# Kernel tuning notes

Hardware: AMD Instinct MI355X
Metric: run time of the kernel (lower is better)

## Reference

```python
import jax, jax.numpy as jnp
import numpy as np

B, N, F, H, E, L = 4, 4096, 256, 256, 262144, 3
NTOT = B * N
EPS = 1e-5
NEG_SLOPE = 0.2  # PyG GATConv default leaky_relu slope


def setup_inputs() -> dict:
    key = jax.random.key(0)
    ks = jax.random.split(key, 10)
    s = 0.05
    return {
        "x": jax.random.normal(ks[0], (B, 1, N, F), jnp.float32),
        "edge_index": jax.random.randint(ks[1], (2, E), 0, NTOT, jnp.int64),
        "tc_w": jax.random.normal(ks[2], (H, F, 3), jnp.float32) * s,   # Conv1d weight [out,in,k]
        "tc_b": jax.random.normal(ks[3], (H,), jnp.float32) * s,
        "gat_W": jax.random.normal(ks[4], (L, H, H), jnp.float32) * s,  # per-layer lin weight (in==hidden)
        "gat_as": jax.random.normal(ks[5], (L, H), jnp.float32) * s,    # att_src
        "gat_ad": jax.random.normal(ks[6], (L, H), jnp.float32) * s,    # att_dst
        "gat_b": jax.random.normal(ks[7], (L, H), jnp.float32) * s,
        "ln_g": jnp.ones((H,), jnp.float32),
        "ln_b": jnp.zeros((H,), jnp.float32),
    }


def _gat_layer(h, W, a_s, a_d, b, src, dst):
    # h: [NTOT, H]; heads=1, eval mode (no dropout), self-loops already in src/dst
    hw = h @ W                                  # [NTOT, H]
    e = jax.nn.leaky_relu((hw @ a_s)[src] + (hw @ a_d)[dst], NEG_SLOPE)  # [E']
    m = jax.ops.segment_max(e, dst, num_segments=NTOT)
    ex = jnp.exp(e - m[dst])
    denom = jax.ops.segment_sum(ex, dst, num_segments=NTOT)
    alpha = ex / denom[dst]                     # edge softmax over incoming edges
    out = jax.ops.segment_sum(alpha[:, None] * hw[src], dst, num_segments=NTOT)
    return out + b


def reference(x, edge_index, tc_w, tc_b, gat_W, gat_as, gat_ad, gat_b, ln_g, ln_b):
    # add self loops (PyG GATConv default add_self_loops=True)
    loops = jnp.arange(NTOT, dtype=edge_index.dtype)
    src = jnp.concatenate([edge_index[0], loops])
    dst = jnp.concatenate([edge_index[1], loops])

    def conv1d(y):  # y: [B, C, N]
        o = jax.lax.conv_general_dilated(y, tc_w, (1,), [(1, 1)],
                                         dimension_numbers=("NCH", "OIH", "NCH"))
        return o + tc_b[None, :, None]

    xt = jnp.transpose(x[:, 0], (0, 2, 1))      # [B, F, N]
    xt = jax.nn.relu(conv1d(xt) + xt)           # temporal conv + residual

    h = jnp.transpose(xt, (0, 2, 1)).reshape(NTOT, H)
    for l in range(L):
        h = jax.nn.relu(_gat_layer(h, gat_W[l], gat_as[l], gat_ad[l], gat_b[l], src, dst))

    hg = jnp.transpose(h.reshape(B, N, H), (0, 2, 1))  # [B, H, N]
    out = conv1d(hg)[:, :, 0]                   # [B, H]

    mu = jnp.mean(out, axis=-1, keepdims=True)
    var = jnp.var(out, axis=-1, keepdims=True)
    out = (out - mu) / jnp.sqrt(var + EPS) * ln_g + ln_b
    return jax.nn.relu(out)
```

## Files before the change

### kernel.cpp

```cpp
#include <hip/hip_runtime.h>
#include <hip/hip_bf16.h>
#include <math.h>

#define NTOT 16384
#define HDIM 256
#define BBATCH 4
#define NSEQ 4096
#define FDIM 256
#define NE 262144
#define NEE (NE + NTOT)
#define NLAYER 3
#define LN_EPS 1e-5f
#define SLOPE 0.2f
#define CAP 64

typedef __attribute__((ext_vector_type(8))) short bf16x8;
typedef __attribute__((ext_vector_type(4))) float f32x4;

#define LDW 80
#define SLDW 72

#define OFF_HA   0u
#define OFF_HW   8388608u
#define OFF_WC   16777216u
#define OFF_WL   17170432u
#define OFF_SP   17563648u
#define OFF_DP   17825792u
#define OFF_CNT  18087936u
#define OFF_CSR  18153472u
#define OFF_WT   22347776u
#define OFF_F1   23134208u
#define OFF_F2   23199744u
#define OFF_L1   23265280u
#define OFF_L2   23330816u
#define OFF_CT   23396352u

static __device__ __forceinline__ unsigned short f2b(float f) {
    __hip_bfloat16 h = __float2bfloat16(f);
    return __builtin_bit_cast(unsigned short, h);
}
static __device__ __forceinline__ float b2f(unsigned short u) {
    __hip_bfloat16 h = __builtin_bit_cast(__hip_bfloat16, u);
    return __bfloat162float(h);
}
static __device__ __forceinline__ float rlanef(float v, int l) {
    return __builtin_bit_cast(float, __builtin_amdgcn_readlane(__builtin_bit_cast(int, v), l));
}

static __device__ __forceinline__ void wave_append(bool isNew, int src, int lane,
                                                   int* ctp, int* list) {
    unsigned long long mask = __ballot(isNew);
    int base = 0;
    if (lane == 0 && mask) base = atomicAdd(ctp, (int)__popcll(mask));
    base = __shfl(base, 0);
    if (isNew) {
        int off = (int)__popcll(mask & ((1ull << lane) - 1ull));
        list[base + off] = src;
    }
}

__global__ __launch_bounds__(256) void k_pre(const float* __restrict__ tcw, const float* __restrict__ gatW,
                                             unsigned short* __restrict__ wcB, unsigned short* __restrict__ WTb,
                                             float* __restrict__ wT, int* __restrict__ cnt,
                                             int* __restrict__ flag1, int* __restrict__ flag2,
                                             int* __restrict__ ct) {
    int b = blockIdx.x, t = threadIdx.x;
    if (b < 256) {
        const float* s = tcw + b * 768 + t * 3;
        wcB[b * 768 + 0 + t]   = f2b(s[0]);
        wcB[b * 768 + 256 + t] = f2b(s[1]);
        wcB[b * 768 + 512 + t] = f2b(s[2]);
    } else if (b < 1024) {
        int ln = b - 256; int n = ln & 255; int l = ln >> 8;
        WTb[(size_t)l * 65536 + n * 256 + t] = f2b(gatW[(size_t)l * 65536 + t * 256 + n]);
    } else if (b < 1792) {
        int fk = b - 1024; int f = fk / 3, k = fk - 3 * f;
        wT[(k * FDIM + f) * HDIM + t] = tcw[t * 768 + fk];
    } else if (b < 1808) {
        int i = ((b - 1792) * 256 + t) * 4;
        *(int4*)(cnt + i) = make_int4(0, 0, 0, 0);
    } else if (b < 1824) {
        int i = ((b - 1808) * 256 + t) * 4;
        *(int4*)(flag1 + i) = make_int4(0, 0, 0, 0);
    } else if (b < 1840) {
        int i = ((b - 1824) * 256 + t) * 4;
        *(int4*)(flag2 + i) = make_int4(0, 0, 0, 0);
    } else {
        if (t < 2) ct[t] = 0;
    }
}

__global__ __launch_bounds__(256) void k_conv(const float* __restrict__ x,
                                              const unsigned short* __restrict__ wcB,
                                              const float* __restrict__ tcb,
                                              unsigned short* __restrict__ hAb,
                                              const int* __restrict__ ei, int* __restrict__ cnt,
                                              int* __restrict__ csr,
                                              int* __restrict__ flag2, int* __restrict__ list2,
                                              int* __restrict__ ct) {
    __shared__ char slab[130 * SLDW];
    __shared__ char Bs[3 * 64 * LDW];
    int t = threadIdx.x;
    if (blockIdx.x >= 128) {
        int cid = (blockIdx.x - 128) * 4 + blockIdx.y;
        int e = cid * 256 + t;
        int src, dst;
        if (e < NE) { src = ei[e]; dst = ei[NE + e]; } else { src = dst = e - NE; }
        int slot = atomicAdd(&cnt[dst], 1);
        if (slot < CAP) csr[dst * CAP + slot] = src;
        bool isNew = false;
        if ((dst & 4095) < 2) isNew = (atomicExch(&flag2[src], 1) == 0);
        wave_append(isNew, src, t & 63, &ct[0], list2);
        return;
    }
    int m0 = blockIdx.x * 128, n0 = blockIdx.y * 64;
    int bb = m0 >> 12;
    int nloc0 = m0 & 4095;
    int w = t >> 6, lane = t & 63;
    int wr = w >> 1, wc = w & 1;
    int row16 = lane & 15, kg = lane >> 4;
    int rA = t >> 1, hh = t & 1;
    f32x4 acc[4][2];
    #pragma unroll
    for (int mi = 0; mi < 4; ++mi)
        #pragma unroll
        for (int ni = 0; ni < 2; ++ni) acc[mi][ni] = (f32x4)(0.f);

    for (int kb = 0; kb < 8; ++kb) {
        int c0 = kb * 32;
        __syncthreads();
        {
            int nl = nloc0 - 1 + rA;
            ushort4 o0 = make_ushort4(0,0,0,0), o1 = make_ushort4(0,0,0,0),
                    o2 = make_ushort4(0,0,0,0), o3 = make_ushort4(0,0,0,0);
            if ((unsigned)nl < 4096u) {
// ... 35 lines not shown
            #pragma unroll
            for (int ni = 0; ni < 2; ++ni)
                bfr[ni] = *(bf16x8*)&Bs[p * 64 * LDW + (wc * 32 + ni * 16 + row16) * LDW + kg * 16];
            #pragma unroll
            for (int mi = 0; mi < 4; ++mi) {
                bf16x8 afr = *(bf16x8*)&slab[(wr * 64 + mi * 16 + row16 + p) * SLDW + kg * 16];
                acc[mi][0] = __builtin_amdgcn_mfma_f32_16x16x32_bf16(afr, bfr[0], acc[mi][0], 0, 0, 0);
                acc[mi][1] = __builtin_amdgcn_mfma_f32_16x16x32_bf16(afr, bfr[1], acc[mi][1], 0, 0, 0);
            }
        }
    }
    #pragma unroll
    for (int mi = 0; mi < 4; ++mi)
        #pragma unroll
        for (int ni = 0; ni < 2; ++ni) {
            int rowl = wr * 64 + mi * 16 + kg * 4;
            int coll = wc * 32 + ni * 16 + row16;
            int n = n0 + coll;
            float bc = tcb[n];
            #pragma unroll
            for (int q = 0; q < 4; ++q) {
                size_t node = (size_t)(m0 + rowl + q);
                float v = acc[mi][ni][q] + bc + x[node * 256 + n];
                v = v > 0.f ? v : 0.f;
                hAb[node * 256 + n] = f2b(v);
            }
        }
}

__global__ __launch_bounds__(256) void k_gemm_layer(const unsigned short* __restrict__ hAb,
                                                    const unsigned short* __restrict__ WT,
                                                    const float* __restrict__ as, const float* __restrict__ ad,
                                                    unsigned short* __restrict__ hwB,
                                                    float* __restrict__ sPart, float* __restrict__ dPart,
                                                    const int* __restrict__ cnt, const int* __restrict__ csr,
                                                    int* __restrict__ flag1,
                                                    int* __restrict__ list1, const int* __restrict__ list2,
                                                    int* __restrict__ ct) {
    __shared__ char lds[128 * LDW + 64 * LDW];
    __shared__ float sRed[256], dRed[256];
    char* As = lds;
    char* Bs = lds + 128 * LDW;
    int t = threadIdx.x;
    if (blockIdx.x == 128) {
        int lane = t & 63;
        int n2 = ct[0];
        int total = n2 * CAP;
        for (int p = blockIdx.y * 256 + t; p < total; p += 1024) {
            int node = list2[p >> 6];
            int j = p & (CAP - 1);
            int src = 0; bool isNew = false;
            if (j < cnt[node]) {
                src = csr[node * CAP + j];
                isNew = (atomicExch(&flag1[src], 1) == 0);
            }
            wave_append(isNew, src, lane, &ct[1], list1);
        }
        return;
    }
    int m0 = blockIdx.x * 128, n0 = blockIdx.y * 64;
    int w = t >> 6, lane = t & 63;
    int wr = w >> 1, wc = w & 1;
    int row16 = lane & 15, kg = lane >> 4;
    int rA = t >> 1, hh = t & 1;
    f32x4 acc[4][2];
    #pragma unroll
    for (int mi = 0; mi < 4; ++mi)
        #pragma unroll
        for (int ni = 0; ni < 2; ++ni) acc[mi][ni] = (f32x4)(0.f);

    for (int kb = 0; kb < 256; kb += 32) {
        {
            const uint4* src = (const uint4*)(hAb + (size_t)(m0 + rA) * 256 + kb + hh * 16);
            uint4 v0 = src[0], v1 = src[1];
            *(uint4*)&As[rA * LDW + hh * 32] = v0;
            *(uint4*)&As[rA * LDW + hh * 32 + 16] = v1;
        }
        if (t < 128) {
            int rB = t >> 1;
            const uint4* src = (const uint4*)(WT + (size_t)(n0 + rB) * 256 + kb + hh * 16);
            uint4 v0 = src[0], v1 = src[1];
            *(uint4*)&Bs[rB * LDW + hh * 32] = v0;
            *(uint4*)&Bs[rB * LDW + hh * 32 + 16] = v1;
        }
        __syncthreads();
        bf16x8 bfr[2];
        #pragma unroll
        for (int ni = 0; ni < 2; ++ni)
            bfr[ni] = *(bf16x8*)&Bs[(wc * 32 + ni * 16 + row16) * LDW + kg * 16];
        #pragma unroll
        for (int mi = 0; mi < 4; ++mi) {
            bf16x8 afr = *(bf16x8*)&As[(wr * 64 + mi * 16 + row16) * LDW + kg * 16];
            acc[mi][0] = __builtin_amdgcn_mfma_f32_16x16x32_bf16(afr, bfr[0], acc[mi][0], 0, 0, 0);
            acc[mi][1] = __builtin_amdgcn_mfma_f32_16x16x32_bf16(afr, bfr[1], acc[mi][1], 0, 0, 0);
        }
        __syncthreads();
    }
    #pragma unroll
    for (int mi = 0; mi < 4; ++mi)
        #pragma unroll
        for (int ni = 0; ni < 2; ++ni) {
            int rowl = wr * 64 + mi * 16 + kg * 4;
            int coll = wc * 32 + ni * 16 + row16;
            size_t base = (size_t)(m0 + rowl) * 256 + n0 + coll;
            #pragma unroll
            for (int q = 0; q < 4; ++q) hwB[base + (size_t)q * 256] = f2b(acc[mi][ni][q]);
        }
    float asv0 = as[n0 + wc * 32 + row16];
    float asv1 = as[n0 + wc * 32 + 16 + row16];
    float adv0 = ad[n0 + wc * 32 + row16];
    float adv1 = ad[n0 + wc * 32 + 16 + row16];
    #pragma unroll
    for (int mi = 0; mi < 4; ++mi)
        #pragma unroll
        for (int q = 0; q < 4; ++q) {
            float ps = acc[mi][0][q] * asv0 + acc[mi][1][q] * asv1;
            float pd = acc[mi][0][q] * adv0 + acc[mi][1][q] * adv1;
            #pragma unroll
            for (int o = 1; o < 16; o <<= 1) { ps += __shfl_xor(ps, o); pd += __shfl_xor(pd, o); }
            if (row16 == 0) {
                int rowl = wr * 64 + mi * 16 + kg * 4 + q;
                sRed[rowl * 2 + wc] = ps;
                dRed[rowl * 2 + wc] = pd;
            }
        }
    __syncthreads();
    if (t < 128) {
        sPart[(size_t)blockIdx.y * NTOT + m0 + t] = sRed[t * 2] + sRed[t * 2 + 1];
        dPart[(size_t)blockIdx.y * NTOT + m0 + t] = dRed[t * 2] + dRed[t * 2 + 1];
    }
}

__global__ __launch_bounds__(256) void k_gemm_list(const unsigned short* __restrict__ hAb,
                                                   const unsigned short* __restrict__ WT,
                                                   const float* __restrict__ as, const float* __restrict__ ad,
                                                   unsigned short* __restrict__ hwB,
                                                   float* __restrict__ sPart, float* __restrict__ dPart,
                                                   const int* __restrict__ list, const int* __restrict__ cptr) {
    __shared__ char lds[128 * LDW + 64 * LDW];
    __shared__ float sRed[256], dRed[256];
    __shared__ int rows[128];
    char* As = lds;
    char* Bs = lds + 128 * LDW;
    int t = threadIdx.x;
    int n = *cptr;
    int m0 = blockIdx.x * 128;
    if (m0 >= n) return;
    int n0 = blockIdx.y * 64;
    if (t < 128) {
        int idx = m0 + t;
        rows[t] = list[idx < n ? idx : n - 1];
    }
    __syncthreads();
    int w = t >> 6, lane = t & 63;
    int wr = w >> 1, wc = w & 1;
    int row16 = lane & 15, kg = lane >> 4;
    int rA = t >> 1, hh = t & 1;
    f32x4 acc[4][2];
    #pragma unroll
    for (int mi = 0; mi < 4; ++mi)
        #pragma unroll
        for (int ni = 0; ni < 2; ++ni) acc[mi][ni] = (f32x4)(0.f);

    for (int kb = 0; kb < 256; kb += 32) {
        {
            const uint4* src = (const uint4*)(hAb + (size_t)rows[rA] * 256 + kb + hh * 16);
            uint4 v0 = src[0], v1 = src[1];
            *(uint4*)&As[rA * LDW + hh * 32] = v0;
            *(uint4*)&As[rA * LDW + hh * 32 + 16] = v1;
        }
        if (t < 128) {
            int rB = t >> 1;
            const uint4* src = (const uint4*)(WT + (size_t)(n0 + rB) * 256 + kb + hh * 16);
            uint4 v0 = src[0], v1 = src[1];
            *(uint4*)&Bs[rB * LDW + hh * 32] = v0;
            *(uint4*)&Bs[rB * LDW + hh * 32 + 16] = v1;
        }
        __syncthreads();
        bf16x8 bfr[2];
        #pragma unroll
        for (int ni = 0; ni < 2; ++ni)
            bfr[ni] = *(bf16x8*)&Bs[(wc * 32 + ni * 16 + row16) * LDW + kg * 16];
        #pragma unroll
        for (int mi = 0; mi < 4; ++mi) {
            bf16x8 afr = *(bf16x8*)&As[(wr * 64 + mi * 16 + row16) * LDW + kg * 16];
            acc[mi][0] = __builtin_amdgcn_mfma_f32_16x16x32_bf16(afr, bfr[0], acc[mi][0], 0, 0, 0);
            acc[mi][1] = __builtin_amdgcn_mfma_f32_16x16x32_bf16(afr, bfr[1], acc[mi][1], 0, 0, 0);
        }
        __syncthreads();
    }
    #pragma unroll
    for (int mi = 0; mi < 4; ++mi)
        #pragma unroll
        for (int ni = 0; ni < 2; ++ni) {
            int rowl = wr * 64 + mi * 16 + kg * 4;
            int coll = wc * 32 + ni * 16 + row16;
            #pragma unroll
            for (int q = 0; q < 4; ++q)
                hwB[(size_t)rows[rowl + q] * 256 + n0 + coll] = f2b(acc[mi][ni][q]);
        }
    float asv0 = as[n0 + wc * 32 + row16];
    float asv1 = as[n0 + wc * 32 + 16 + row16];
    float adv0 = ad[n0 + wc * 32 + row16];
    float adv1 = ad[n0 + wc * 32 + 16 + row16];
    #pragma unroll
    for (int mi = 0; mi < 4; ++mi)
        #pragma unroll
        for (int q = 0; q < 4; ++q) {
            float ps = acc[mi][0][q] * asv0 + acc[mi][1][q] * asv1;
            float pd = acc[mi][0][q] * adv0 + acc[mi][1][q] * adv1;
            #pragma unroll
            for (int o = 1; o < 16; o <<= 1) { ps += __shfl_xor(ps, o); pd += __shfl_xor(pd, o); }
            if (row16 == 0) {
                int rowl = wr * 64 + mi * 16 + kg * 4 + q;
                sRed[rowl * 2 + wc] = ps;
                dRed[rowl * 2 + wc] = pd;
            }
        }
    __syncthreads();
    if (t < 128) {
        int node = rows[t];
        sPart[(size_t)blockIdx.y * NTOT + node] = sRed[t * 2] + sRed[t * 2 + 1];
        dPart[(size_t)blockIdx.y * NTOT + node] = dRed[t * 2] + dRed[t * 2 + 1];
    }
}

__global__ __launch_bounds__(256) void k_agg_list(const unsigned short* __restrict__ hwB,
                                                  const float* __restrict__ sPart, const float* __restrict__ dPart,
                                                  const int* __restrict__ cnt, const int* __restrict__ csr,
                                                  const float* __restrict__ bias,
                                                  unsigned short* __restrict__ hout,
                                                  const int* __restrict__ list, const int* __restrict__ cptr) {
    int tid = threadIdx.x;
    int wave = tid >> 6, lane = tid & 63;
    int n = *cptr;
    const ushort4* hw4 = (const ushort4*)hwB;
    for (int idx = blockIdx.x * 4 + wave; idx < n; idx += gridDim.x * 4) {
        int node = list[idx];
        int deg = cnt[node];
        const int* bucket = csr + node * CAP;
        float di = dPart[node] + dPart[NTOT + node] + dPart[2 * NTOT + node] + dPart[3 * NTOT + node];
        float denom = 0.f;
        float a0 = 0.f, a1 = 0.f, a2 = 0.f, a3 = 0.f;
        for (int cb = 0; cb < deg; cb += 64) {
            int j = cb + lane;
            int sj = 0;
            float myw = 0.f;
            if (j < deg) {
                sj = bucket[j];
                float sv = sPart[sj] + sPart[NTOT + sj] + sPart[2 * NTOT + sj] + sPart[3 * NTOT + sj];
                float e = sv + di;
                e = e > 0.f ? e : SLOPE * e;
                myw = __expf(e);
            }
            float csum = myw;
            #pragma unroll
            for (int o = 1; o < 64; o <<= 1) csum += __shfl_xor(csum, o);
            denom += csum;
            int c = deg - cb; if (c > 64) c = 64;
            int q = 0;
            for (; q + 8 <= c; q += 8) {
                int si[8]; float wi[8]; ushort4 vv[8];
                #pragma unroll
                for (int u = 0; u < 8; ++u) {
                    si[u] = __builtin_amdgcn_readlane(sj, q + u);
                    wi[u] = rlanef(myw, q + u);
                }
                #pragma unroll
                for (int u = 0; u < 8; ++u) vv[u] = hw4[(size_t)si[u] * 64 + lane];
                #pragma unroll
                for (int u = 0; u < 8; ++u) {
                    a0 = fmaf(wi[u], b2f(vv[u].x), a0);
                    a1 = fmaf(wi[u], b2f(vv[u].y), a1);
                    a2 = fmaf(wi[u], b2f(vv[u].z), a2);
                    a3 = fmaf(wi[u], b2f(vv[u].w), a3);
                }
            }
            if (q < c) {
                int rem = c - q;
                int si[8]; float wi[8]; ushort4 vv[8];
                #pragma unroll
                for (int u = 0; u < 8; ++u) {
                    int qq = q + (u < rem ? u : 0);
                    si[u] = __builtin_amdgcn_readlane(sj, qq);
                    wi[u] = (u < rem) ? rlanef(myw, qq) : 0.f;
                }
                #pragma unroll
                for (int u = 0; u < 8; ++u) vv[u] = hw4[(size_t)si[u] * 64 + lane];
                #pragma unroll
                for (int u = 0; u < 8; ++u) {
                    a0 = fmaf(wi[u], b2f(vv[u].x), a0);
                    a1 = fmaf(wi[u], b2f(vv[u].y), a1);
                    a2 = fmaf(wi[u], b2f(vv[u].z), a2);
                    a3 = fmaf(wi[u], b2f(vv[u].w), a3);
                }
            }
        }
        float inv = 1.f / denom;
        float4 bb = ((const float4*)bias)[lane];
        ushort4 o;
        float o0 = a0 * inv + bb.x; o.x = f2b(o0 > 0.f ? o0 : 0.f);
        float o1 = a1 * inv + bb.y; o.y = f2b(o1 > 0.f ? o1 : 0.f);
        float o2 = a2 * inv + bb.z; o.z = f2b(o2 > 0.f ? o2 : 0.f);
        float o3 = a3 * inv + bb.w; o.w = f2b(o3 > 0.f ? o3 : 0.f);
        ((ushort4*)hout)[(size_t)node * 64 + lane] = o;
    }
}

__global__ __launch_bounds__(256) void k_aggfinal(const unsigned short* __restrict__ hwB,
                                                  const float* __restrict__ sPart, const float* __restrict__ dPart,
                                                  const int* __restrict__ cnt, const int* __restrict__ csr,
                                                  const float* __restrict__ bias,
                                                  const float* __restrict__ wT, const float* __restrict__ tcb,
                                                  const float* __restrict__ g, const float* __restrict__ bln,
                                                  float* __restrict__ out) {
    __shared__ float r01[2][HDIM];
    __shared__ float red[16];
    int b = blockIdx.x, t = threadIdx.x;
    int w = t >> 6, lane = t & 63;
    if (w < 2) {
        int node = b * NSEQ + w;
        int deg = cnt[node];
        const int* bucket = csr + node * CAP;
        float di = dPart[node] + dPart[NTOT + node] + dPart[2 * NTOT + node] + dPart[3 * NTOT + node];
        const ushort4* hw4 = (const ushort4*)hwB;
        float denom = 0.f;
        float a0 = 0.f, a1 = 0.f, a2 = 0.f, a3 = 0.f;
        for (int cb = 0; cb < deg; cb += 64) {
            int j = cb + lane;
            int sj = 0;
            float myw = 0.f;
            if (j < deg) {
                sj = bucket[j];
                float sv = sPart[sj] + sPart[NTOT + sj] + sPart[2 * NTOT + sj] + sPart[3 * NTOT + sj];
                float e = sv + di;
                e = e > 0.f ? e : SLOPE * e;
                myw = __expf(e);
            }
            float csum = myw;
            #pragma unroll
            for (int o = 1; o < 64; o <<= 1) csum += __shfl_xor(csum, o);
            denom += csum;
            int c = deg - cb; if (c > 64) c = 64;
            for (int q = 0; q < c; ++q) {
                int sq = __builtin_amdgcn_readlane(sj, q);
                float wq = rlanef(myw, q);
                ushort4 v = hw4[(size_t)sq * 64 + lane];
                a0 = fmaf(wq, b2f(v.x), a0); a1 = fmaf(wq, b2f(v.y), a1);
                a2 = fmaf(wq, b2f(v.z), a2); a3 = fmaf(wq, b2f(v.w), a3);
            }
        }
        float inv = 1.f / denom;
        float4 bb = ((const float4*)bias)[lane];
        float o0 = a0 * inv + bb.x;
        float o1 = a1 * inv + bb.y;
        float o2 = a2 * inv + bb.z;
        float o3 = a3 * inv + bb.w;
        r01[w][lane * 4 + 0] = o0 > 0.f ? o0 : 0.f;
        r01[w][lane * 4 + 1] = o1 > 0.f ? o1 : 0.f;
        r01[w][lane * 4 + 2] = o2 > 0.f ? o2 : 0.f;
        r01[w][lane * 4 + 3] = o3 > 0.f ? o3 : 0.f;
    }
    __syncthreads();
    int c = t;
    float a = tcb[c];
    for (int f = 0; f < FDIM; ++f) {
        a = fmaf(wT[(1 * FDIM + f) * HDIM + c], r01[0][f], a);
        a = fmaf(wT[(2 * FDIM + f) * HDIM + c], r01[1][f], a);
    }
    float ss = a, sq = a * a;
    #pragma unroll
    for (int o = 1; o < 64; o <<= 1) { ss += __shfl_xor(ss, o); sq += __shfl_xor(sq, o); }
    if (lane == 0) { red[w] = ss; red[8 + w] = sq; }
    __syncthreads();
    float tot = 0.f, totq = 0.f;
    #pragma unroll
    for (int u = 0; u < 4; ++u) { tot += red[u]; totq += red[8 + u]; }
    float mu = tot * (1.f / HDIM);
    float var = totq * (1.f / HDIM) - mu * mu;
    float v = (a - mu) * rsqrtf(var + LN_EPS) * g[c] + bln[c];
    out[b * HDIM + c] = v > 0.f ? v : 0.f;
}

extern "C" void kernel_launch(void* const* d_in, const int* in_sizes, int n_in,
                              void* d_out, int out_size, void* d_ws, size_t ws_size,
                              hipStream_t stream) {
    const float* x     = (const float*)d_in[0];
    const int*   ei    = (const int*)d_in[1];
    const float* tcw   = (const float*)d_in[2];
    const float* tcb   = (const float*)d_in[3];
    const float* gatW  = (const float*)d_in[4];
    const float* gatas = (const float*)d_in[5];
    const float* gatad = (const float*)d_in[6];
    const float* gatb  = (const float*)d_in[7];
    const float* lng   = (const float*)d_in[8];
    const float* lnb   = (const float*)d_in[9];
    float* out = (float*)d_out;

    char* ws = (char*)d_ws;
    unsigned short* hAb = (unsigned short*)(ws + OFF_HA);
    unsigned short* hwB = (unsigned short*)(ws + OFF_HW);
    unsigned short* wcB = (unsigned short*)(ws + OFF_WC);
    unsigned short* WTb = (unsigned short*)(ws + OFF_WL);
    float* sPart = (float*)(ws + OFF_SP);
    float* dPart = (float*)(ws + OFF_DP);
    int*   cnt  = (int*)(ws + OFF_CNT);
    int*   csr  = (int*)(ws + OFF_CSR);
    float* wT   = (float*)(ws + OFF_WT);
    int*   flag1 = (int*)(ws + OFF_F1);
    int*   flag2 = (int*)(ws + OFF_F2);
    int*   list1 = (int*)(ws + OFF_L1);
    int*   list2 = (int*)(ws + OFF_L2);
    int*   ct    = (int*)(ws + OFF_CT);

    k_pre<<<1841, 256, 0, stream>>>(tcw, gatW, wcB, WTb, wT, cnt, flag1, flag2, ct);
    k_conv<<<dim3(128 + 272, 4), 256, 0, stream>>>(x, wcB, tcb, hAb, ei, cnt, csr,
                                                   flag2, list2, ct);

    k_gemm_layer<<<dim3(129, 4), 256, 0, stream>>>(
        hAb, WTb, gatas, gatad, hwB, sPart, dPart,
        cnt, csr, flag1, list1, list2, ct);
    k_agg_list<<<1024, 256, 0, stream>>>(hwB, sPart, dPart, cnt, csr, gatb, hAb, list1, ct + 1);

    k_gemm_list<<<dim3(128, 4), 256, 0, stream>>>(
        hAb, WTb + 65536, gatas + HDIM, gatad + HDIM, hwB, sPart, dPart, list1, ct + 1);
    k_agg_list<<<128, 256, 0, stream>>>(hwB, sPart, dPart, cnt, csr, gatb + HDIM, hAb, list2, ct);

    k_gemm_list<<<dim3(4, 4), 256, 0, stream>>>(
        hAb, WTb + 131072, gatas + 2 * HDIM, gatad + 2 * HDIM, hwB, sPart, dPart, list2, ct);
    k_aggfinal<<<BBATCH, 256, 0, stream>>>(hwB, sPart, dPart, cnt, csr, gatb + 2 * HDIM,
                                           wT, tcb, lng, lnb, out);
}
```

Before: 117.5 us.

## Fuse GAT tail layers into one cooperative kernel with grid syncs

Replaces the chain of per-layer aggregation and list-GEMM kernels, plus the final aggregation and LayerNorm kernel, with a single cooperative kernel of 256 blocks. The stages inside it are separated by grid.sync, and aggregation and GEMM work is spread over the list entries with grid-stride loops. Weight transposes and the flag1 clear move from the prep kernel into spare blocks of the conv kernel, and the layer-0 GEMM no longer builds the second frontier list. The intent is to remove kernel launch gaps and tail latency on the small frontier stages. In exchange, building list1 is no longer overlapped with the layer-0 GEMM, and each grid-wide barrier adds its own cost.

```diff
diff --git a/kernel.cpp b/kernel.cpp
--- a/kernel.cpp
+++ b/kernel.cpp
@@ -1,6 +1,9 @@
 #include <hip/hip_runtime.h>
 #include <hip/hip_bf16.h>
+#include <hip/hip_cooperative_groups.h>
 #include <math.h>
+
+namespace cg = cooperative_groups;
 
 #define NTOT 16384
 #define HDIM 256
@@ -9,7 +12,6 @@
 #define FDIM 256
 #define NE 262144
 #define NEE (NE + NTOT)
-#define NLAYER 3
 #define LN_EPS 1e-5f
 #define SLOPE 0.2f
 #define CAP 64
@@ -59,10 +61,182 @@
     }
 }
 
-__global__ __launch_bounds__(256) void k_pre(const float* __restrict__ tcw, const float* __restrict__ gatW,
-                                             unsigned short* __restrict__ wcB, unsigned short* __restrict__ WTb,
-                                             float* __restrict__ wT, int* __restrict__ cnt,
-                                             int* __restrict__ flag1, int* __restrict__ flag2,
+static __device__ __forceinline__ float4 agg_node(const unsigned short* __restrict__ hwB,
+                                                  const float* __restrict__ sPart,
+                                                  const float* __restrict__ dPart,
+                                                  const int* __restrict__ cnt,
+                                                  const int* __restrict__ csr,
+                                                  const float* __restrict__ bias,
+                                                  int node, int lane) {
+    int deg = cnt[node];
+    const int* bucket = csr + node * CAP;
+    float di = dPart[node] + dPart[NTOT + node] + dPart[2 * NTOT + node] + dPart[3 * NTOT + node];
+    const ushort4* hw4 = (const ushort4*)hwB;
+    float denom = 0.f;
+    float a0 = 0.f, a1 = 0.f, a2 = 0.f, a3 = 0.f;
+    for (int cb = 0; cb < deg; cb += 64) {
+        int j = cb + lane;
+        int sj = 0;
+        float myw = 0.f;
+        if (j < deg) {
+            sj = bucket[j];
+            float sv = sPart[sj] + sPart[NTOT + sj] + sPart[2 * NTOT + sj] + sPart[3 * NTOT + sj];
+            float e = sv + di;
+            e = e > 0.f ? e : SLOPE * e;
+            myw = __expf(e);
+        }
+        float csum = myw;
+        #pragma unroll
+        for (int o = 1; o < 64; o <<= 1) csum += __shfl_xor(csum, o);
+        denom += csum;
+        int c = deg - cb; if (c > 64) c = 64;
+        int q = 0;
+        for (; q + 8 <= c; q += 8) {
+            int si[8]; float wi[8]; ushort4 vv[8];
+            #pragma unroll
+            for (int u = 0; u < 8; ++u) {
+                si[u] = __builtin_amdgcn_readlane(sj, q + u);
+                wi[u] = rlanef(myw, q + u);
+            }
+            #pragma unroll
+            for (int u = 0; u < 8; ++u) vv[u] = hw4[(size_t)si[u] * 64 + lane];
+            #pragma unroll
+            for (int u = 0; u < 8; ++u) {
+                a0 = fmaf(wi[u], b2f(vv[u].x), a0);
+                a1 = fmaf(wi[u], b2f(vv[u].y), a1);
+                a2 = fmaf(wi[u], b2f(vv[u].z), a2);
+                a3 = fmaf(wi[u], b2f(vv[u].w), a3);
+            }
+        }
+        if (q < c) {
+            int rem = c - q;
+            int si[8]; float wi[8]; ushort4 vv[8];
+            #pragma unroll
+            for (int u = 0; u < 8; ++u) {
+                int qq = q + (u < rem ? u : 0);
+                si[u] = __builtin_amdgcn_readlane(sj, qq);
+                wi[u] = (u < rem) ? rlanef(myw, qq) : 0.f;
+            }
+            #pragma unroll
+            for (int u = 0; u < 8; ++u) vv[u] = hw4[(size_t)si[u] * 64 + lane];
+            #pragma unroll
+            for (int u = 0; u < 8; ++u) {
+                a0 = fmaf(wi[u], b2f(vv[u].x), a0);
+                a1 = fmaf(wi[u], b2f(vv[u].y), a1);
+                a2 = fmaf(wi[u], b2f(vv[u].z), a2);
+                a3 = fmaf(wi[u], b2f(vv[u].w), a3);
+            }
+        }
+    }
+    float inv = 1.f / denom;
+    float4 bb = ((const float4*)bias)[lane];
+    float4 o;
+    o.x = a0 * inv + bb.x; o.x = o.x > 0.f ? o.x : 0.f;
+    o.y = a1 * inv + bb.y; o.y = o.y > 0.f ? o.y : 0.f;
+    o.z = a2 * inv + bb.z; o.z = o.z > 0.f ? o.z : 0.f;
+    o.w = a3 * inv + bb.w; o.w = o.w > 0.f ? o.w : 0.f;
+    return o;
+}
+
+static __device__ __forceinline__ void gemm_tile(const unsigned short* __restrict__ hAb,
+                                                 const unsigned short* __restrict__ WT,
+                                                 const float* __restrict__ as, const float* __restrict__ ad,
+                                                 unsigned short* __restrict__ hwB,
+                                                 float* __restrict__ sPart, float* __restrict__ dPart,
+                                                 const int* __restrict__ list, int n, int m0, int n0,
+                                                 char* As, char* Bs, float* sRed, float* dRed, int* rows) {
+    int t = threadIdx.x;
+    __syncthreads();
+    if (t < 128) {
+        int idx = m0 + t;
+        rows[t] = list[idx < n ? idx : n - 1];
+    }
+    __syncthreads();
+    int w = t >> 6, lane = t & 63;
+    int wr = w >> 1, wc = w & 1;
+    int row16 = lane & 15, kg = lane >> 4;
+    int rA = t >> 1, hh = t & 1;
+    f32x4 acc[4][2];
+    #pragma unroll
+    for (int mi = 0; mi < 4; ++mi)
+        #pragma unroll
+        for (int ni = 0; ni < 2; ++ni) acc[mi][ni] = (f32x4)(0.f);
+
+    for (int kb = 0; kb < 256; kb += 32) {
+        {
+            const uint4* src = (const uint4*)(hAb + (size_t)rows[rA] * 256 + kb + hh * 16);
+            uint4 v0 = src[0], v1 = src[1];
+            *(uint4*)&As[rA * LDW + hh * 32] = v0;
+            *(uint4*)&As[rA * LDW + hh * 32 + 16] = v1;
+        }
+        if (t < 128) {
+            int rB = t >> 1;
+            const uint4* src = (const uint4*)(WT + (size_t)(n0 + rB) * 256 + kb + hh * 16);
+            uint4 v0 = src[0], v1 = src[1];
+            *(uint4*)&Bs[rB * LDW + hh * 32] = v0;
+            *(uint4*)&Bs[rB * LDW + hh * 32 + 16] = v1;
+        }
+        __syncthreads();
+        bf16x8 bfr[2];
+        #pragma unroll
+        for (int ni = 0; ni < 2; ++ni)
+            bfr[ni] = *(bf16x8*)&Bs[(wc * 32 + ni * 16 + row16) * LDW + kg * 16];
+        #pragma unroll
+        for (int mi = 0; mi < 4; ++mi) {
+            bf16x8 afr = *(bf16x8*)&As[(wr * 64 + mi * 16 + row16) * LDW + kg * 16];
+            acc[mi][0] = __builtin_amdgcn_mfma_f32_16x16x32_bf16(afr, bfr[0], acc[mi][0], 0, 0, 0);
+            acc[mi][1] = __builtin_amdgcn_mfma_f32_16x16x32_bf16(afr, bfr[1], acc[mi][1], 0, 0, 0);
+        }
+        __syncthreads();
+    }
+    #pragma unroll
+    for (int mi = 0; mi < 4; ++mi)
+        #pragma unroll
+        for (int ni = 0; ni < 2; ++ni) {
+            int rowl = wr * 64 + mi * 16 + kg * 4;
+            int coll = wc * 32 + ni * 16 + row16;
+            #pragma unroll
+            for (int q = 0; q < 4; ++q)
+                hwB[(size_t)rows[rowl + q] * 256 + n0 + coll] = f2b(acc[mi][ni][q]);
+        }
+    float asv0 = as[n0 + wc * 32 + row16];
+    float asv1 = as[n0 + wc * 32 + 16 + row16];
+    float adv0 = ad[n0 + wc * 32 + row16];
+    float adv1 = ad[n0 + wc * 32 + 16 + row16];
+    #pragma unroll
+    for (int mi = 0; mi < 4; ++mi)
+        #pragma unroll
+        for (int q = 0; q < 4; ++q) {
+            float ps = acc[mi][0][q] * asv0 + acc[mi][1][q] * asv1;
+            float pd = acc[mi][0][q] * adv0 + acc[mi][1][q] * adv1;
+            #pragma unroll
+            for (int o = 1; o < 16; o <<= 1) { ps += __shfl_xor(ps, o); pd += __shfl_xor(pd, o); }
+            if (row16 == 0) {
+                int rowl = wr * 64 + mi * 16 + kg * 4 + q;
+                sRed[rowl * 2 + wc] = ps;
+                dRed[rowl * 2 + wc] = pd;
+            }
+        }
+    __syncthreads();
+    if (t < 128) {
+        int node = rows[t];
+        sPart[(size_t)blockIdx.y * 0 + 0 * NTOT + node] = sRed[t * 2] + sRed[t * 2 + 1];
+        dPart[node] = dRed[t * 2] + dRed[t * 2 + 1];
+    }
+}
+
+static __device__ __forceinline__ void gemm_tile_sd(const unsigned short* hAb, const unsigned short* WT,
+                                                    const float* as, const float* ad,
+                                                    unsigned short* hwB, float* sPart, float* dPart,
+                                                    const int* list, int n, int m0, int n0,
+                                                    char* As, char* Bs, float* sRed, float* dRed, int* rows) {
+    gemm_tile(hAb, WT, as, ad, hwB, sPart + (size_t)(n0 >> 6) * NTOT, dPart + (size_t)(n0 >> 6) * NTOT,
+              list, n, m0, n0, As, Bs, sRed, dRed, rows);
+}
+
+__global__ __launch_bounds__(256) void k_pre(const float* __restrict__ tcw,
+                                             unsigned short* __restrict__ wcB,
+                                             int* __restrict__ cnt, int* __restrict__ flag2,
                                              int* __restrict__ ct) {
     int b = blockIdx.x, t = threadIdx.x;
     if (b < 256) {
@@ -70,20 +244,11 @@
         wcB[b * 768 + 0 + t]   = f2b(s[0]);
         wcB[b * 768 + 256 + t] = f2b(s[1]);
         wcB[b * 768 + 512 + t] = f2b(s[2]);
-    } else if (b < 1024) {
-        int ln = b - 256; int n = ln & 255; int l = ln >> 8;
-        WTb[(size_t)l * 65536 + n * 256 + t] = f2b(gatW[(size_t)l * 65536 + t * 256 + n]);
-    } else if (b < 1792) {
-        int fk = b - 1024; int f = fk / 3, k = fk - 3 * f;
-        wT[(k * FDIM + f) * HDIM + t] = tcw[t * 768 + fk];
-    } else if (b < 1808) {
-        int i = ((b - 1792) * 256 + t) * 4;
+    } else if (b < 272) {
+        int i = ((b - 256) * 256 + t) * 4;
         *(int4*)(cnt + i) = make_int4(0, 0, 0, 0);
-    } else if (b < 1824) {
-        int i = ((b - 1808) * 256 + t) * 4;
-        *(int4*)(flag1 + i) = make_int4(0, 0, 0, 0);
-    } else if (b < 1840) {
-        int i = ((b - 1824) * 256 + t) * 4;
+    } else if (b < 288) {
+        int i = ((b - 272) * 256 + t) * 4;
         *(int4*)(flag2 + i) = make_int4(0, 0, 0, 0);
     } else {
         if (t < 2) ct[t] = 0;
@@ -97,10 +262,27 @@
                                               const int* __restrict__ ei, int* __restrict__ cnt,
                                               int* __restrict__ csr,
                                               int* __restrict__ flag2, int* __restrict__ list2,
-                                              int* __restrict__ ct) {
+                                              int* __restrict__ ct,
+                                              const float* __restrict__ tcw, const float* __restrict__ gatW,
+                                              unsigned short* __restrict__ WTb, float* __restrict__ wT,
+                                              int* __restrict__ flag1) {
     __shared__ char slab[130 * SLDW];
     __shared__ char Bs[3 * 64 * LDW];
     int t = threadIdx.x;
+    if (blockIdx.x >= 400) {
+        int pid = (blockIdx.x - 400) * 4 + blockIdx.y;
+        if (pid < 768) {
+            int l = pid >> 8, n = pid & 255;
+            WTb[(size_t)l * 65536 + n * 256 + t] = f2b(gatW[(size_t)l * 65536 + t * 256 + n]);
+        } else if (pid < 1536) {
+            int fk = pid - 768; int f = fk / 3, k = fk - 3 * f;
+            wT[(k * FDIM + f) * HDIM + t] = tcw[t * 768 + fk];
+        } else {
+            int i = ((pid - 1536) * 256 + t) * 4;
+            *(int4*)(flag1 + i) = make_int4(0, 0, 0, 0);
+        }
+        return;
+    }
     if (blockIdx.x >= 128) {
         int cid = (blockIdx.x - 128) * 4 + blockIdx.y;
         int e = cid * 256 + t;
@@ -202,21 +384,108 @@
                                                     const unsigned short* __restrict__ WT,
                                                     const float* __restrict__ as, const float* __restrict__ ad,
                                                     unsigned short* __restrict__ hwB,
-                                                    float* __restrict__ sPart, float* __restrict__ dPart,
-                                                    const int* __restrict__ cnt, const int* __restrict__ csr,
-                                                    int* __restrict__ flag1,
-                                                    int* __restrict__ list1, const int* __restrict__ list2,
-                                                    int* __restrict__ ct) {
+                                                    float* __restrict__ sPart, float* __restrict__ dPart) {
     __shared__ char lds[128 * LDW + 64 * LDW];
     __shared__ float sRed[256], dRed[256];
     char* As = lds;
     char* Bs = lds + 128 * LDW;
     int t = threadIdx.x;
-    if (blockIdx.x == 128) {
-        int lane = t & 63;
+    int m0 = blockIdx.x * 128, n0 = blockIdx.y * 64;
+    int w = t >> 6, lane = t & 63;
+    int wr = w >> 1, wc = w & 1;
+    int row16 = lane & 15, kg = lane >> 4;
+    int rA = t >> 1, hh = t & 1;
+    f32x4 acc[4][2];
+    #pragma unroll
+    for (int mi = 0; mi < 4; ++mi)
+        #pragma unroll
+        for (int ni = 0; ni < 2; ++ni) acc[mi][ni] = (f32x4)(0.f);
+
+    for (int kb = 0; kb < 256; kb += 32) {
+        {
+            const uint4* src = (const uint4*)(hAb + (size_t)(m0 + rA) * 256 + kb + hh * 16);
+            uint4 v0 = src[0], v1 = src[1];
+            *(uint4*)&As[rA * LDW + hh * 32] = v0;
+            *(uint4*)&As[rA * LDW + hh * 32 + 16] = v1;
+        }
+        if (t < 128) {
+            int rB = t >> 1;
+            const uint4* src = (const uint4*)(WT + (size_t)(n0 + rB) * 256 + kb + hh * 16);
+            uint4 v0 = src[0], v1 = src[1];
+            *(uint4*)&Bs[rB * LDW + hh * 32] = v0;
+            *(uint4*)&Bs[rB * LDW + hh * 32 + 16] = v1;
+        }
+        __syncthreads();
+        bf16x8 bfr[2];
+        #pragma unroll
+        for (int ni = 0; ni < 2; ++ni)
+            bfr[ni] = *(bf16x8*)&Bs[(wc * 32 + ni * 16 + row16) * LDW + kg * 16];
+        #pragma unroll
+        for (int mi = 0; mi < 4; ++mi) {
+            bf16x8 afr = *(bf16x8*)&As[(wr * 64 + mi * 16 + row16) * LDW + kg * 16];
+            acc[mi][0] = __builtin_amdgcn_mfma_f32_16x16x32_bf16(afr, bfr[0], acc[mi][0], 0, 0, 0);
+            acc[mi][1] = __builtin_amdgcn_mfma_f32_16x16x32_bf16(afr, bfr[1], acc[mi][1], 0, 0, 0);
+        }
+        __syncthreads();
+    }
+    #pragma unroll
+    for (int mi = 0; mi < 4; ++mi)
+        #pragma unroll
+        for (int ni = 0; ni < 2; ++ni) {
+            int rowl = wr * 64 + mi * 16 + kg * 4;
+            int coll = wc * 32 + ni * 16 + row16;
+            size_t base = (size_t)(m0 + rowl) * 256 + n0 + coll;
+            #pragma unroll
+            for (int q = 0; q < 4; ++q) hwB[base + (size_t)q * 256] = f2b(acc[mi][ni][q]);
+        }
+    float asv0 = as[n0 + wc * 32 + row16];
+    float asv1 = as[n0 + wc * 32 + 16 + row16];
+    float adv0 = ad[n0 + wc * 32 + row16];
+    float adv1 = ad[n0 + wc * 32 + 16 + row16];
+    #pragma unroll
+    for (int mi = 0; mi < 4; ++mi)
+        #pragma unroll
+        for (int q = 0; q < 4; ++q) {
+            float ps = acc[mi][0][q] * asv0 + acc[mi][1][q] * asv1;
+            float pd = acc[mi][0][q] * adv0 + acc[mi][1][q] * adv1;
+            #pragma unroll
+            for (int o = 1; o < 16; o <<= 1) { ps += __shfl_xor(ps, o); pd += __shfl_xor(pd, o); }
+            if (row16 == 0) {
+                int rowl = wr * 64 + mi * 16 + kg * 4 + q;
+                sRed[rowl * 2 + wc] = ps;
+                dRed[rowl * 2 + wc] = pd;
+            }
+        }
+    __syncthreads();
+    if (t < 128) {
+        sPart[(size_t)blockIdx.y * NTOT + m0 + t] = sRed[t * 2] + sRed[t * 2 + 1];
+        dPart[(size_t)blockIdx.y * NTOT + m0 + t] = dRed[t * 2] + dRed[t * 2 + 1];
+    }
+}
+
+__global__ __launch_bounds__(256) void k_tail(unsigned short* hAb, unsigned short* hwB,
+                                              const unsigned short* WTb,
+                                              const float* gatas, const float* gatad, const float* gatb,
+                                              float* sPart, float* dPart,
+                                              const int* cnt, const int* csr,
+                                              int* flag1, int* list1, const int* list2, int* ct,
+                                              const float* wT, const float* tcb,
+                                              const float* g, const float* bln, float* out) {
+    cg::grid_group grid = cg::this_grid();
+    __shared__ char As[128 * LDW];
+    __shared__ char Bs[64 * LDW];
+    __shared__ float sRed[256], dRed[256];
+    __shared__ int rows[128];
+    __shared__ float r01[2][HDIM];
+    __shared__ float red[16];
+    int b = blockIdx.x, t = threadIdx.x;
+    int wv = t >> 6, lane = t & 63;
+    int nb = gridDim.x;
+
+    if (b < 4) {
         int n2 = ct[0];
         int total = n2 * CAP;
-        for (int p = blockIdx.y * 256 + t; p < total; p += 1024) {
+        for (int p = b * 256 + t; p < total; p += 1024) {
             int node = list2[p >> 6];
             int j = p & (CAP - 1);
             int src = 0; bool isNew = false;
@@ -226,330 +495,74 @@
             }
             wave_append(isNew, src, lane, &ct[1], list1);
         }
-        return;
-    }
-    int m0 = blockIdx.x * 128, n0 = blockIdx.y * 64;
-    int w = t >> 6, lane = t & 63;
-    int wr = w >> 1, wc = w & 1;
-    int row16 = lane & 15, kg = lane >> 4;
-    int rA = t >> 1, hh = t & 1;
-    f32x4 acc[4][2];
-    #pragma unroll
-    for (int mi = 0; mi < 4; ++mi)
-        #pragma unroll
-        for (int ni = 0; ni < 2; ++ni) acc[mi][ni] = (f32x4)(0.f);
-
-    for (int kb = 0; kb < 256; kb += 32) {
-        {
-            const uint4* src = (const uint4*)(hAb + (size_t)(m0 + rA) * 256 + kb + hh * 16);
-            uint4 v0 = src[0], v1 = src[1];
-            *(uint4*)&As[rA * LDW + hh * 32] = v0;
-            *(uint4*)&As[rA * LDW + hh * 32 + 16] = v1;
-        }
-        if (t < 128) {
-            int rB = t >> 1;
-            const uint4* src = (const uint4*)(WT + (size_t)(n0 + rB) * 256 + kb + hh * 16);
-            uint4 v0 = src[0], v1 = src[1];
-            *(uint4*)&Bs[rB * LDW + hh * 32] = v0;
-            *(uint4*)&Bs[rB * LDW + hh * 32 + 16] = v1;
-        }
-        __syncthreads();
-        bf16x8 bfr[2];
-        #pragma unroll
-        for (int ni = 0; ni < 2; ++ni)
-            bfr[ni] = *(bf16x8*)&Bs[(wc * 32 + ni * 16 + row16) * LDW + kg * 16];
-        #pragma unroll
-        for (int mi = 0; mi < 4; ++mi) {
-            bf16x8 afr = *(bf16x8*)&As[(wr * 64 + mi * 16 + row16) * LDW + kg * 16];
-            acc[mi][0] = __builtin_amdgcn_mfma_f32_16x16x32_bf16(afr, bfr[0], acc[mi][0], 0, 0, 0);
-            acc[mi][1] = __builtin_amdgcn_mfma_f32_16x16x32_bf16(afr, bfr[1], acc[mi][1], 0, 0, 0);
-        }
-        __syncthreads();
-    }
-    #pragma unroll
-    for (int mi = 0; mi < 4; ++mi)
-        #pragma unroll
-        for (int ni = 0; ni < 2; ++ni) {
-            int rowl = wr * 64 + mi * 16 + kg * 4;
-            int coll = wc * 32 + ni * 16 + row16;
-            size_t base = (size_t)(m0 + rowl) * 256 + n0 + coll;
-            #pragma unroll
-            for (int q = 0; q < 4; ++q) hwB[base + (size_t)q * 256] = f2b(acc[mi][ni][q]);
-        }
-    float asv0 = as[n0 + wc * 32 + row16];
-    float asv1 = as[n0 + wc * 32 + 16 + row16];
-    float adv0 = ad[n0 + wc * 32 + row16];
-    float adv1 = ad[n0 + wc * 32 + 16 + row16];
-    #pragma unroll
-    for (int mi = 0; mi < 4; ++mi)
-        #pragma unroll
-        for (int q = 0; q < 4; ++q) {
-            float ps = acc[mi][0][q] * asv0 + acc[mi][1][q] * asv1;
-            float pd = acc[mi][0][q] * adv0 + acc[mi][1][q] * adv1;
-            #pragma unroll
-            for (int o = 1; o < 16; o <<= 1) { ps += __shfl_xor(ps, o); pd += __shfl_xor(pd, o); }
-            if (row16 == 0) {
-                int rowl = wr * 64 + mi * 16 + kg * 4 + q;
-                sRed[rowl * 2 + wc] = ps;
-                dRed[rowl * 2 + wc] = pd;
-            }
-        }
-    __syncthreads();
-    if (t < 128) {
-        sPart[(size_t)blockIdx.y * NTOT + m0 + t] = sRed[t * 2] + sRed[t * 2 + 1];
-        dPart[(size_t)blockIdx.y * NTOT + m0 + t] = dRed[t * 2] + dRed[t * 2 + 1];
-    }
-}
-
-__global__ __launch_bounds__(256) void k_gemm_list(const unsigned short* __restrict__ hAb,
-                                                   const unsigned short* __restrict__ WT,
-                                                   const float* __restrict__ as, const float* __restrict__ ad,
-                                                   unsigned short* __restrict__ hwB,
-                                                   float* __restrict__ sPart, float* __restrict__ dPart,
-                                                   const int* __restrict__ list, const int* __restrict__ cptr) {
-    __shared__ char lds[128 * LDW + 64 * LDW];
-    __shared__ float sRed[256], dRed[256];
-    __shared__ int rows[128];
-    char* As = lds;
-    char* Bs = lds + 128 * LDW;
-    int t = threadIdx.x;
-    int n = *cptr;
-    int m0 = blockIdx.x * 128;
-    if (m0 >= n) return;
-    int n0 = blockIdx.y * 64;
-    if (t < 128) {
-        int idx = m0 + t;
-        rows[t] = list[idx < n ? idx : n - 1];
-    }
-    __syncthreads();
-    int w = t >> 6, lane = t & 63;
-    int wr = w >> 1, wc = w & 1;
-    int row16 = lane & 15, kg = lane >> 4;
-    int rA = t >> 1, hh = t & 1;
-    f32x4 acc[4][2];
-    #pragma unroll
-    for (int mi = 0; mi < 4; ++mi)
-        #pragma unroll
-        for (int ni = 0; ni < 2; ++ni) acc[mi][ni] = (f32x4)(0.f);
-
-    for (int kb = 0; kb < 256; kb += 32) {
-        {
-            const uint4* src = (const uint4*)(hAb + (size_t)rows[rA] * 256 + kb + hh * 16);
-            uint4 v0 = src[0], v1 = src[1];
-            *(uint4*)&As[rA * LDW + hh * 32] = v0;
-            *(uint4*)&As[rA * LDW + hh * 32 + 16] = v1;
-        }
-        if (t < 128) {
-            int rB = t >> 1;
-            const uint4* src = (const uint4*)(WT + (size_t)(n0 + rB) * 256 + kb + hh * 16);
-            uint4 v0 = src[0], v1 = src[1];
-            *(uint4*)&Bs[rB * LDW + hh * 32] = v0;
-            *(uint4*)&Bs[rB * LDW + hh * 32 + 16] = v1;
-        }
-        __syncthreads();
-        bf16x8 bfr[2];
-        #pragma unroll
-        for (int ni = 0; ni < 2; ++ni)
-            bfr[ni] = *(bf16x8*)&Bs[(wc * 32 + ni * 16 + row16) * LDW + kg * 16];
-        #pragma unroll
-        for (int mi = 0; mi < 4; ++mi) {
-            bf16x8 afr = *(bf16x8*)&As[(wr * 64 + mi * 16 + row16) * LDW + kg * 16];
-            acc[mi][0] = __builtin_amdgcn_mfma_f32_16x16x32_bf16(afr, bfr[0], acc[mi][0], 0, 0, 0);
-            acc[mi][1] = __builtin_amdgcn_mfma_f32_16x16x32_bf16(afr, bfr[1], acc[mi][1], 0, 0, 0);
-        }
-        __syncthreads();
-    }
-    #pragma unroll
-    for (int mi = 0; mi < 4; ++mi)
-        #pragma unroll
-        for (int ni = 0; ni < 2; ++ni) {
-            int rowl = wr * 64 + mi * 16 + kg * 4;
-            int coll = wc * 32 + ni * 16 + row16;
-            #pragma unroll
-            for (int q = 0; q < 4; ++q)
-                hwB[(size_t)rows[rowl + q] * 256 + n0 + coll] = f2b(acc[mi][ni][q]);
-        }
-    float asv0 = as[n0 + wc * 32 + row16];
-    float asv1 = as[n0 + wc * 32 + 16 + row16];
-    float adv0 = ad[n0 + wc * 32 + row16];
-    float adv1 = ad[n0 + wc * 32 + 16 + row16];
-    #pragma unroll
-    for (int mi = 0; mi < 4; ++mi)
-        #pragma unroll
-        for (int q = 0; q < 4; ++q) {
-            float ps = acc[mi][0][q] * asv0 + acc[mi][1][q] * asv1;
-            float pd = acc[mi][0][q] * adv0 + acc[mi][1][q] * adv1;
-            #pragma unroll
-            for (int o = 1; o < 16; o <<= 1) { ps += __shfl_xor(ps, o); pd += __shfl_xor(pd, o); }
-            if (row16 == 0) {
-                int rowl = wr * 64 + mi * 16 + kg * 4 + q;
-                sRed[rowl * 2 + wc] = ps;
-                dRed[rowl * 2 + wc] = pd;
-            }
-        }
-    __syncthreads();
-    if (t < 128) {
-        int node = rows[t];
-        sPart[(size_t)blockIdx.y * NTOT + node] = sRed[t * 2] + sRed[t * 2 + 1];
-        dPart[(size_t)blockIdx.y * NTOT + node] = dRed[t * 2] + dRed[t * 2 + 1];
-    }
-}
-
-__global__ __launch_bounds__(256) void k_agg_list(const unsigned short* __restrict__ hwB,
-                                                  const float* __restrict__ sPart, const float* __restrict__ dPart,
-                                                  const int* __restrict__ cnt, const int* __restrict__ csr,
-                                                  const float* __restrict__ bias,
-                                                  unsigned short* __restrict__ hout,
-                                                  const int* __restrict__ list, const int* __restrict__ cptr) {
-    int tid = threadIdx.x;
-    int wave = tid >> 6, lane = tid & 63;
-    int n = *cptr;
-    const ushort4* hw4 = (const ushort4*)hwB;
-    for (int idx = blockIdx.x * 4 + wave; idx < n; idx += gridDim.x * 4) {
-        int node = list[idx];
-        int deg = cnt[node];
-        const int* bucket = csr + node * CAP;
-        float di = dPart[node] + dPart[NTOT + node] + dPart[2 * NTOT + node] + dPart[3 * NTOT + node];
-        float denom = 0.f;
-        float a0 = 0.f, a1 = 0.f, a2 = 0.f, a3 = 0.f;
-        for (int cb = 0; cb < deg; cb += 64) {
-            int j = cb + lane;
-            int sj = 0;
-            float myw = 0.f;
-            if (j < deg) {
-                sj = bucket[j];
-                float sv = sPart[sj] + sPart[NTOT + sj] + sPart[2 * NTOT + sj] + sPart[3 * NTOT + sj];
-                float e = sv + di;
-                e = e > 0.f ? e : SLOPE * e;
-                myw = __expf(e);
-            }
-            float csum = myw;
-            #pragma unroll
-            for (int o = 1; o < 64; o <<= 1) csum += __shfl_xor(csum, o);
-            denom += csum;
-            int c = deg - cb; if (c > 64) c = 64;
-            int q = 0;
-            for (; q + 8 <= c; q += 8) {
-                int si[8]; float wi[8]; ushort4 vv[8];
-                #pragma unroll
-                for (int u = 0; u < 8; ++u) {
-                    si[u] = __builtin_amdgcn_readlane(sj, q + u);
-                    wi[u] = rlanef(myw, q + u);
-                }
-                #pragma unroll
-                for (int u = 0; u < 8; ++u) vv[u] = hw4[(size_t)si[u] * 64 + lane];
-                #pragma unroll
-                for (int u = 0; u < 8; ++u) {
-                    a0 = fmaf(wi[u], b2f(vv[u].x), a0);
-                    a1 = fmaf(wi[u], b2f(vv[u].y), a1);
-                    a2 = fmaf(wi[u], b2f(vv[u].z), a2);
-                    a3 = fmaf(wi[u], b2f(vv[u].w), a3);
-                }
-            }
-            if (q < c) {
-                int rem = c - q;
-                int si[8]; float wi[8]; ushort4 vv[8];
-                #pragma unroll
-                for (int u = 0; u < 8; ++u) {
-                    int qq = q + (u < rem ? u : 0);
-                    si[u] = __builtin_amdgcn_readlane(sj, qq);
-                    wi[u] = (u < rem) ? rlanef(myw, qq) : 0.f;
-                }
-                #pragma unroll
-                for (int u = 0; u < 8; ++u) vv[u] = hw4[(size_t)si[u] * 64 + lane];
-                #pragma unroll
-                for (int u = 0; u < 8; ++u) {
-                    a0 = fmaf(wi[u], b2f(vv[u].x), a0);
-                    a1 = fmaf(wi[u], b2f(vv[u].y), a1);
-                    a2 = fmaf(wi[u], b2f(vv[u].z), a2);
-                    a3 = fmaf(wi[u], b2f(vv[u].w), a3);
-                }
-            }
-        }
-        float inv = 1.f / denom;
-        float4 bb = ((const float4*)bias)[lane];
-        ushort4 o;
-        float o0 = a0 * inv + bb.x; o.x = f2b(o0 > 0.f ? o0 : 0.f);
-        float o1 = a1 * inv + bb.y; o.y = f2b(o1 > 0.f ? o1 : 0.f);
-        float o2 = a2 * inv + bb.z; o.z = f2b(o2 > 0.f ? o2 : 0.f);
-        float o3 = a3 * inv + bb.w; o.w = f2b(o3 > 0.f ? o3 : 0.f);
-        ((ushort4*)hout)[(size_t)node * 64 + lane] = o;
-    }
-}
-
-__global__ __launch_bounds__(256) void k_aggfinal(const unsigned short* __restrict__ hwB,
-                                                  const float* __restrict__ sPart, const float* __restrict__ dPart,
-                                                  const int* __restrict__ cnt, const int* __restrict__ csr,
-                                                  const float* __restrict__ bias,
-                                                  const float* __restrict__ wT, const float* __restrict__ tcb,
-                                                  const float* __restrict__ g, const float* __restrict__ bln,
-                                                  float* __restrict__ out) {
-    __shared__ float r01[2][HDIM];
-    __shared__ float red[16];
-    int b = blockIdx.x, t = threadIdx.x;
-    int w = t >> 6, lane = t & 63;
-    if (w < 2) {
-        int node = b * NSEQ + w;
-        int deg = cnt[node];
-        const int* bucket = csr + node * CAP;
-        float di = dPart[node] + dPart[NTOT + node] + dPart[2 * NTOT + node] + dPart[3 * NTOT + node];
-        const ushort4* hw4 = (const ushort4*)hwB;
-        float denom = 0.f;
-        float a0 = 0.f, a1 = 0.f, a2 = 0.f, a3 = 0.f;
-        for (int cb = 0; cb < deg; cb += 64) {
-            int j = cb + lane;
-            int sj = 0;
-            float myw = 0.f;
-            if (j < deg) {
-                sj = bucket[j];
-                float sv = sPart[sj] + sPart[NTOT + sj] + sPart[2 * NTOT + sj] + sPart[3 * NTOT + sj];
-                float e = sv + di;
-                e = e > 0.f ? e : SLOPE * e;
-                myw = __expf(e);
-            }
-            float csum = myw;
-            #pragma unroll
-            for (int o = 1; o < 64; o <<= 1) csum += __shfl_xor(csum, o);
-            denom += csum;
-            int c = deg - cb; if (c > 64) c = 64;
-            for (int q = 0; q < c; ++q) {
-                int sq = __builtin_amdgcn_readlane(sj, q);
-                float wq = rlanef(myw, q);
-                ushort4 v = hw4[(size_t)sq * 64 + lane];
-                a0 = fmaf(wq, b2f(v.x), a0); a1 = fmaf(wq, b2f(v.y), a1);
-                a2 = fmaf(wq, b2f(v.z), a2); a3 = fmaf(wq, b2f(v.w), a3);
-            }
-        }
-        float inv = 1.f / denom;
-        float4 bb = ((const float4*)bias)[lane];
-        float o0 = a0 * inv + bb.x;
-        float o1 = a1 * inv + bb.y;
-        float o2 = a2 * inv + bb.z;
-        float o3 = a3 * inv + bb.w;
-        r01[w][lane * 4 + 0] = o0 > 0.f ? o0 : 0.f;
-        r01[w][lane * 4 + 1] = o1 > 0.f ? o1 : 0.f;
-        r01[w][lane * 4 + 2] = o2 > 0.f ? o2 : 0.f;
-        r01[w][lane * 4 + 3] = o3 > 0.f ? o3 : 0.f;
-    }
-    __syncthreads();
-    int c = t;
-    float a = tcb[c];
-    for (int f = 0; f < FDIM; ++f) {
-        a = fmaf(wT[(1 * FDIM + f) * HDIM + c], r01[0][f], a);
-        a = fmaf(wT[(2 * FDIM + f) * HDIM + c], r01[1][f], a);
-    }
-    float ss = a, sq = a * a;
-    #pragma unroll
-    for (int o = 1; o < 64; o <<= 1) { ss += __shfl_xor(ss, o); sq += __shfl_xor(sq, o); }
-    if (lane == 0) { red[w] = ss; red[8 + w] = sq; }
-    __syncthreads();
-    float tot = 0.f, totq = 0.f;
-    #pragma unroll
-    for (int u = 0; u < 4; ++u) { tot += red[u]; totq += red[8 + u]; }
-    float mu = tot * (1.f / HDIM);
-    float var = totq * (1.f / HDIM) - mu * mu;
-    float v = (a - mu) * rsqrtf(var + LN_EPS) * g[c] + bln[c];
-    out[b * HDIM + c] = v > 0.f ? v : 0.f;
+    }
+    grid.sync();
+    int n1 = ct[1];
+    int n2 = ct[0];
+
+    for (int idx = b * 4 + wv; idx < n1; idx += nb * 4) {
+        int node = list1[idx];
+        float4 o = agg_node(hwB, sPart, dPart, cnt, csr, gatb, node, lane);
+        ushort4 u;
+        u.x = f2b(o.x); u.y = f2b(o.y); u.z = f2b(o.z); u.w = f2b(o.w);
+        ((ushort4*)hAb)[(size_t)node * 64 + lane] = u;
+    }
+    grid.sync();
+
+    {
+        int ntiles = ((n1 + 127) >> 7) * 4;
+        for (int tile = b; tile < ntiles; tile += nb)
+            gemm_tile_sd(hAb, WTb + 65536, gatas + HDIM, gatad + HDIM, hwB, sPart, dPart,
+                         list1, n1, (tile >> 2) * 128, (tile & 3) * 64, As, Bs, sRed, dRed, rows);
+    }
+    grid.sync();
+
+    for (int idx = b * 4 + wv; idx < n2; idx += nb * 4) {
+        int node = list2[idx];
+        float4 o = agg_node(hwB, sPart, dPart, cnt, csr, gatb + HDIM, node, lane);
+        ushort4 u;
+        u.x = f2b(o.x); u.y = f2b(o.y); u.z = f2b(o.z); u.w = f2b(o.w);
+        ((ushort4*)hAb)[(size_t)node * 64 + lane] = u;
+    }
+    grid.sync();
+
+    {
+        int ntiles = ((n2 + 127) >> 7) * 4;
+        for (int tile = b; tile < ntiles; tile += nb)
+            gemm_tile_sd(hAb, WTb + 131072, gatas + 2 * HDIM, gatad + 2 * HDIM, hwB, sPart, dPart,
+                         list2, n2, (tile >> 2) * 128, (tile & 3) * 64, As, Bs, sRed, dRed, rows);
+    }
+    grid.sync();
+
+    if (b < BBATCH) {
+        if (wv < 2) {
+            int node = b * NSEQ + wv;
+            float4 o = agg_node(hwB, sPart, dPart, cnt, csr, gatb + 2 * HDIM, node, lane);
+            r01[wv][lane * 4 + 0] = o.x;
+            r01[wv][lane * 4 + 1] = o.y;
+            r01[wv][lane * 4 + 2] = o.z;
+            r01[wv][lane * 4 + 3] = o.w;
+        }
+        __syncthreads();
+        int c = t;
+        float a = tcb[c];
+        for (int f = 0; f < FDIM; ++f) {
+            a = fmaf(wT[(1 * FDIM + f) * HDIM + c], r01[0][f], a);
+            a = fmaf(wT[(2 * FDIM + f) * HDIM + c], r01[1][f], a);
+        }
+        float ss = a, sq = a * a;
+        #pragma unroll
+        for (int o = 1; o < 64; o <<= 1) { ss += __shfl_xor(ss, o); sq += __shfl_xor(sq, o); }
+        if (lane == 0) { red[wv] = ss; red[8 + wv] = sq; }
+        __syncthreads();
+        float tot = 0.f, totq = 0.f;
+        #pragma unroll
+        for (int u = 0; u < 4; ++u) { tot += red[u]; totq += red[8 + u]; }
+        float mu = tot * (1.f / HDIM);
+        float var = totq * (1.f / HDIM) - mu * mu;
+        float v = (a - mu) * rsqrtf(var + LN_EPS) * g[c] + bln[c];
+        out[b * HDIM + c] = v > 0.f ? v : 0.f;
+    }
 }
 
 extern "C" void kernel_launch(void* const* d_in, const int* in_sizes, int n_in,
@@ -583,21 +596,14 @@
     int*   list2 = (int*)(ws + OFF_L2);
     int*   ct    = (int*)(ws + OFF_CT);
 
-    k_pre<<<1841, 256, 0, stream>>>(tcw, gatW, wcB, WTb, wT, cnt, flag1, flag2, ct);
-    k_conv<<<dim3(128 + 272, 4), 256, 0, stream>>>(x, wcB, tcb, hAb, ei, cnt, csr,
-                                                   flag2, list2, ct);
-
-    k_gemm_layer<<<dim3(129, 4), 256, 0, stream>>>(
-        hAb, WTb, gatas, gatad, hwB, sPart, dPart,
-        cnt, csr, flag1, list1, list2, ct);
-    k_agg_list<<<1024, 256, 0, stream>>>(hwB, sPart, dPart, cnt, csr, gatb, hAb, list1, ct + 1);
-
-    k_gemm_list<<<dim3(128, 4), 256, 0, stream>>>(
-        hAb, WTb + 65536, gatas + HDIM, gatad + HDIM, hwB, sPart, dPart, list1, ct + 1);
-    k_agg_list<<<128, 256, 0, stream>>>(hwB, sPart, dPart, cnt, csr, gatb + HDIM, hAb, list2, ct);
-
-    k_gemm_list<<<dim3(4, 4), 256, 0, stream>>>(
-        hAb, WTb + 131072, gatas + 2 * HDIM, gatad + 2 * HDIM, hwB, sPart, dPart, list2, ct);
-    k_aggfinal<<<BBATCH, 256, 0, stream>>>(hwB, sPart, dPart, cnt, csr, gatb + 2 * HDIM,
-                                           wT, tcb, lng, lnb, out);
-}
+    k_pre<<<289, 256, 0, stream>>>(tcw, wcB, cnt, flag2, ct);
+    k_conv<<<dim3(128 + 272 + 388, 4), 256, 0, stream>>>(x, wcB, tcb, hAb, ei, cnt, csr,
+                                                         flag2, list2, ct, tcw, gatW, WTb, wT, flag1);
+    k_gemm_layer<<<dim3(128, 4), 256, 0, stream>>>(hAb, WTb, gatas, gatad, hwB, sPart, dPart);
+
+    void* args[] = {&hAb, &hwB, &WTb, &gatas, &gatad, &gatb, &sPart, &dPart,
+                    &cnt, &csr, &flag1, &list1, &list2, &ct, &wT, &tcb,
+                    (void*)&lng, (void*)&lnb, &out};
+    hipLaunchCooperativeKernel(reinterpret_cast<void*>(k_tail), dim3(256), dim3(256),
+                               args, 0, stream);
+}
```

New measurement: 247.3 us. 2.1x slower.
